# Performance work log

Measured on AMD Instinct MI355X. Metric: run time of the kernel, lower is better.

The kernel has to match this reference:

```python
import jax, jax.numpy as jnp
import numpy as np
import math

D_MODEL = 1024
NUM_HEADS = 16
D_K = D_MODEL // NUM_HEADS
MAX_SEQ_LEN = 2048
THETA = 10000.0
BATCH = 2
SEQ = 2048


def setup_inputs() -> dict:
    key = jax.random.key(0)
    ks = jax.random.split(key, 5)
    std = math.sqrt(2.0 / (D_MODEL + D_MODEL))
    def w(k):
        return jnp.clip(std * jax.random.normal(k, (D_MODEL, D_MODEL), dtype=jnp.float32), -3 * std, 3 * std)
    return {
        "x": jax.random.normal(ks[0], (BATCH, SEQ, D_MODEL), dtype=jnp.float32),
        "token_positions": jnp.arange(SEQ, dtype=jnp.int32),
        "Wq": w(ks[1]),
        "Wk": w(ks[2]),
        "Wv": w(ks[3]),
        "Wo": w(ks[4]),
    }


def _rope_tables():
    inv_freq = 1.0 / THETA ** (jnp.arange(0, D_K, 2, dtype=jnp.float32) / D_K)  # [d_k/2]
    positions = jnp.arange(MAX_SEQ_LEN, dtype=jnp.float32)[:, None]             # [max_seq, 1]
    angles = positions * inv_freq                                               # [max_seq, d_k/2]
    return jnp.cos(angles), jnp.sin(angles)


def _apply_rope(x, cos, sin):
    # x: [..., seq, d_k]; cos/sin: [seq, d_k/2] (broadcast over leading dims)
    x1, x2 = x[..., ::2], x[..., 1::2]
    r1 = x1 * cos - x2 * sin
    r2 = x1 * sin + x2 * cos
    return jnp.stack((r1, r2), axis=-1).reshape(x.shape)


def reference(x, token_positions, Wq, Wk, Wv, Wo):
    B, S, D = x.shape
    def proj(W):
        y = jnp.einsum('bsd,od->bso', x, W)
        return y.reshape(B, S, NUM_HEADS, D_K).transpose(0, 2, 1, 3)  # [B,H,S,dk]
    q, k, v = proj(Wq), proj(Wk), proj(Wv)

    cos_t, sin_t = _rope_tables()
    cos, sin = cos_t[token_positions], sin_t[token_positions]  # [S, d_k/2]
    q = _apply_rope(q, cos, sin)
    k = _apply_rope(k, cos, sin)

    scores = jnp.einsum('bhqd,bhkd->bhqk', q, k) / math.sqrt(D_K)
    causal = jnp.tril(jnp.ones((S, S), dtype=bool))
    scores = jnp.where(causal, scores, -jnp.inf)
    attn = jax.nn.softmax(scores, axis=-1)
    out = jnp.einsum('bhqk,bhkd->bhqd', attn, v)
    out = out.transpose(0, 2, 1, 3).reshape(B, S, D)
    return jnp.einsum('bsd,od->bso', out, Wo)
```

## Files before the change

### kernel.cpp

```cpp
#include <hip/hip_runtime.h>
#include <hip/hip_bf16.h>


typedef __attribute__((ext_vector_type(8))) short short8;
typedef __attribute__((ext_vector_type(4))) float floatx4;

static __device__ __forceinline__ unsigned short f2bf(float f) {
  __hip_bfloat16 h = __float2bfloat16(f);
  return *(unsigned short*)&h;
}

static __device__ __forceinline__ void gl2lds16(const unsigned short* g,
                                                unsigned short* l) {
  __builtin_amdgcn_global_load_lds(
      (const __attribute__((address_space(1))) void*)g,
      (__attribute__((address_space(3))) void*)l, 16, 0, 0);
}

__global__ __launch_bounds__(256) void cvt_all(
    const float4* __restrict__ x,  const float4* __restrict__ wq,
    const float4* __restrict__ wk, const float4* __restrict__ wv,
    const float4* __restrict__ wo,
    ushort4* __restrict__ xb,  ushort4* __restrict__ wqb,
    ushort4* __restrict__ wkb, ushort4* __restrict__ wvb,
    ushort4* __restrict__ wob,
    const int* __restrict__ tokpos,
    float* __restrict__ ctab, float* __restrict__ stab) {
  int t = blockIdx.y;
  int i = blockIdx.x * 256 + threadIdx.x;
  if (t == 5) {
    if (i < 65536) {
      int s = i >> 5, f = i & 31;
      float inv = expf(-9.210340371976184f * (float)(2 * f) / 64.0f);
      float ang = (float)tokpos[s] * inv;
      ctab[i] = cosf(ang);
      stab[i] = sinf(ang);
    }
    return;
  }
  const float4* s = (t == 0) ? x : (t == 1) ? wq : (t == 2) ? wk : (t == 3) ? wv : wo;
  ushort4* d = (t == 0) ? xb : (t == 1) ? wqb : (t == 2) ? wkb : (t == 3) ? wvb : wob;
  int n4 = (t == 0) ? 1048576 : 262144;
  if (i < n4) {
    float4 v = s[i];
    ushort4 o;
    o.x = f2bf(v.x); o.y = f2bf(v.y); o.z = f2bf(v.z); o.w = f2bf(v.w);
    d[i] = o;
  }
}

#define GEMM128_BODY(Aptr, Wptr, m0, n0)                                        \
  __shared__ __align__(16) unsigned short lA[128 * 64];                         \
  __shared__ __align__(16) unsigned short lB[128 * 64];                         \
  int tid = threadIdx.x;                                                        \
  int wave = tid >> 6, lane = tid & 63;                                         \
  int wm = wave >> 1, wn = wave & 1;                                            \
  int l15 = lane & 15, quad = lane >> 4;                                        \
  int srow = wave * 32 + (lane >> 3);                   \
  int sch = lane & 7;                                   \
  int fsw = l15 & 7;                                 \
  floatx4 acc[4][4];                                                            \
  _Pragma("unroll") for (int m = 0; m < 4; ++m)                                 \
      _Pragma("unroll") for (int n = 0; n < 4; ++n)                             \
          acc[m][n] = (floatx4){0.f, 0.f, 0.f, 0.f};                            \
  for (int kt = 0; kt < 16; ++kt) {                                             \
    _Pragma("unroll") for (int p = 0; p < 4; ++p) {                             \
      int r = srow + p * 8;                                                     \
      int g = sch ^ (r & 7);                                                    \
      gl2lds16(Aptr + (size_t)(m0 + r) * 1024 + kt * 64 + g * 8,                \
               lA + (wave * 32 + p * 8) * 64);                                  \
      gl2lds16(Wptr + (size_t)(n0 + r) * 1024 + kt * 64 + g * 8,                \
               lB + (wave * 32 + p * 8) * 64);                                  \
    }                                                                           \
    __syncthreads();                                                            \
    _Pragma("unroll") for (int ks = 0; ks < 2; ++ks) {                          \
      short8 af[4], bf[4];                                                      \
      _Pragma("unroll") for (int m = 0; m < 4; ++m)                             \
          af[m] = *(const short8*)(lA + (wm * 64 + m * 16 + l15) * 64 +         \
                                   (((ks * 4 + quad) ^ fsw) * 8));              \
      _Pragma("unroll") for (int n = 0; n < 4; ++n)                             \
          bf[n] = *(const short8*)(lB + (wn * 64 + n * 16 + l15) * 64 +         \
                                   (((ks * 4 + quad) ^ fsw) * 8));              \
      _Pragma("unroll") for (int m = 0; m < 4; ++m)                             \
          _Pragma("unroll") for (int n = 0; n < 4; ++n)                         \
              acc[m][n] = __builtin_amdgcn_mfma_f32_16x16x32_bf16(              \
                  af[m], bf[n], acc[m][n], 0, 0, 0);                            \
    }                                                                           \
    __syncthreads();                                                            \
  }

__global__ __launch_bounds__(256) void qkv_mfma(
    const unsigned short* __restrict__ X,
    const unsigned short* __restrict__ Wq,
    const unsigned short* __restrict__ Wk,
    const unsigned short* __restrict__ Wv,
    const float* __restrict__ ctab, const float* __restrict__ stab,
    unsigned short* __restrict__ Qo, unsigned short* __restrict__ Ko,
    unsigned short* __restrict__ Vo) {
  int mat = blockIdx.z;
  const unsigned short* W = (mat == 0) ? Wq : ((mat == 1) ? Wk : Wv);
  unsigned short* Out = (mat == 0) ? Qo : ((mat == 1) ? Ko : Vo);
  int m0 = blockIdx.x * 128, n0 = blockIdx.y * 128;

  GEMM128_BODY(X, W, m0, n0)

#pragma unroll
  for (int n = 0; n < 4; ++n) {
    int col = n0 + wn * 64 + n * 16 + l15;
    int h = col >> 6;
    int d = col & 63;
    int pi = d >> 1;
    bool odd = (d & 1) != 0;
    size_t hb = (size_t)h * 2048 * 64;
#pragma unroll
    for (int m = 0; m < 4; ++m) {
      int row0 = m0 + wm * 64 + m * 16 + quad * 4;
      int b = row0 >> 11;
      int s0 = row0 & 2047;
      size_t base = (size_t)b * 16 * 2048 * 64 + hb;
      if (mat == 2) {
        ushort4 pv;
        pv.x = f2bf(acc[m][n][0]);
        pv.y = f2bf(acc[m][n][1]);
        pv.z = f2bf(acc[m][n][2]);
        pv.w = f2bf(acc[m][n][3]);
        *(ushort4*)(Out + base + (size_t)d * 2048 + s0) = pv;
      } else {
#pragma unroll
        for (int i = 0; i < 4; ++i) {
          int s = s0 + i;
          float v = acc[m][n][i];
          float p = __shfl_xor(v, 1);
          float c = ctab[s * 32 + pi];
          float sn = stab[s * 32 + pi];
          float res = odd ? fmaf(p, sn, v * c) : fmaf(v, c, -p * sn);
          if (mat == 0) res *= 0.1803368801111204f;
          Out[base + (size_t)s * 64 + d] = f2bf(res);
        }
      }
    }
  }
}

__global__ __launch_bounds__(256) void oproj_mfma(
    const unsigned short* __restrict__ A, const unsigned short* __restrict__ Wo,
    float* __restrict__ Out) {
  int m0 = blockIdx.x * 128, n0 = blockIdx.y * 128;

  GEMM128_BODY(A, Wo, m0, n0)

#pragma unroll
  for (int m = 0; m < 4; ++m) {
#pragma unroll
    for (int n = 0; n < 4; ++n) {
      int col = n0 + wn * 64 + n * 16 + l15;
#pragma unroll
      for (int i = 0; i < 4; ++i) {
        int row = m0 + wm * 64 + m * 16 + quad * 4 + i;
        Out[(size_t)row * 1024 + col] = acc[m][n][i];
      }
    }
  }
}

#define LPS 72

__global__ __launch_bounds__(256) void attn_flash(
    const unsigned short* __restrict__ Q, const unsigned short* __restrict__ K,
    const unsigned short* __restrict__ Vt, unsigned short* __restrict__ Oc) {
  __shared__ __align__(16) unsigned short lK[64 * 64];
  __shared__ __align__(16) unsigned short lV[64 * 64];
  __shared__ unsigned short lP[4][16 * LPS];

  int tid = threadIdx.x;
  int wave = tid >> 6, lane = tid & 63;
  int l15 = lane & 15, quad = lane >> 4;

  int xb_ = blockIdx.x;
  int yb_ = blockIdx.y;
  int jb = yb_ >> 3, ib = yb_ & 7;
  int qtile;
  if (jb == 0)      qtile = xb_;
  else if (jb == 1) qtile = 31 - xb_;
  else if (jb == 2) qtile = (15 - xb_) & 31;
  else              qtile = (16 + xb_) & 31;
  int bh = ib * 4 + jb;

  size_t base = (size_t)bh * 2048 * 64;
  int qbase = qtile * 64;

  const unsigned short* qrow = Q + base + (size_t)(qbase + wave * 16 + l15) * 64;
  short8 qb0 = *(const short8*)(qrow + quad * 8);
  short8 qb1 = *(const short8*)(qrow + 32 + quad * 8);

  floatx4 o[4];
  float m_i = -1e30f, l_i = 0.f;
#pragma unroll
  for (int n = 0; n < 4; ++n) o[n] = (floatx4){0.f, 0.f, 0.f, 0.f};

  int r0 = tid >> 3, g = tid & 7;
  int r1 = r0 + 32;
  int e0 = g * 8;
  int sl = (g ^ (r0 & 7)) * 8;
  int fsw = l15 & 7;
  int c0 = (quad ^ fsw) * 8;
  int c1 = ((quad + 4) ^ fsw) * 8;

  const unsigned short* kp = K + base;
  const unsigned short* vp = Vt + base;
  short8 pk0 = *(const short8*)(kp + r0 * 64 + e0);
  short8 pk1 = *(const short8*)(kp + r1 * 64 + e0);
  short8 pv0 = *(const short8*)(vp + (size_t)r0 * 2048 + e0);
  short8 pv1 = *(const short8*)(vp + (size_t)r1 * 2048 + e0);

  for (int kt = 0; kt <= qtile; ++kt) {
    __syncthreads();
    *(short8*)(lK + r0 * 64 + sl) = pk0;
    *(short8*)(lK + r1 * 64 + sl) = pk1;
    *(short8*)(lV + r0 * 64 + sl) = pv0;
    *(short8*)(lV + r1 * 64 + sl) = pv1;
    __syncthreads();

    if (kt < qtile) {
      const unsigned short* kn = K + base + (size_t)(kt + 1) * 64 * 64;
      const unsigned short* vn = Vt + base + (kt + 1) * 64;
      pk0 = *(const short8*)(kn + r0 * 64 + e0);
      pk1 = *(const short8*)(kn + r1 * 64 + e0);
      pv0 = *(const short8*)(vn + (size_t)r0 * 2048 + e0);
      pv1 = *(const short8*)(vn + (size_t)r1 * 2048 + e0);
    }

    float sc[4][4];
#pragma unroll
    for (int sub = 0; sub < 4; ++sub) {
      const unsigned short* kr = lK + (sub * 16 + l15) * 64;
      short8 a0 = *(const short8*)(kr + c0);
      short8 a1 = *(const short8*)(kr + c1);
      floatx4 s = {0.f, 0.f, 0.f, 0.f};
      s = __builtin_amdgcn_mfma_f32_16x16x32_bf16(a0, qb0, s, 0, 0, 0);
      s = __builtin_amdgcn_mfma_f32_16x16x32_bf16(a1, qb1, s, 0, 0, 0);
#pragma unroll
      for (int i = 0; i < 4; ++i) sc[sub][i] = s[i];
    }

    if (kt == qtile) {
      int qin = wave * 16 + l15;
#pragma unroll
      for (int sub = 0; sub < 4; ++sub)
#pragma unroll
        for (int i = 0; i < 4; ++i)
          if (sub * 16 + quad * 4 + i > qin) sc[sub][i] = -1e30f;
    }

    float mb = sc[0][0];
#pragma unroll
    for (int sub = 0; sub < 4; ++sub)
#pragma unroll
      for (int i = 0; i < 4; ++i) mb = fmaxf(mb, sc[sub][i]);
    mb = fmaxf(mb, __shfl_xor(mb, 16));
    mb = fmaxf(mb, __shfl_xor(mb, 32));

    float mn = fmaxf(m_i, mb);
    float al = exp2f(m_i - mn);
    m_i = mn;
    float rs = 0.f;
#pragma unroll
    for (int sub = 0; sub < 4; ++sub)
#pragma unroll
      for (int i = 0; i < 4; ++i) {
        float p = exp2f(sc[sub][i] - mn);
        sc[sub][i] = p;
        rs += p;
      }
    rs += __shfl_xor(rs, 16);
    rs += __shfl_xor(rs, 32);
    l_i = l_i * al + rs;

#pragma unroll
    for (int n = 0; n < 4; ++n) {
      o[n][0] *= al; o[n][1] *= al; o[n][2] *= al; o[n][3] *= al;
    }

    unsigned short* pw = lP[wave];
#pragma unroll
    for (int sub = 0; sub < 4; ++sub) {
      ushort4 pq;
      pq.x = f2bf(sc[sub][0]); pq.y = f2bf(sc[sub][1]);
      pq.z = f2bf(sc[sub][2]); pq.w = f2bf(sc[sub][3]);
      *(ushort4*)(pw + l15 * LPS + sub * 16 + quad * 4) = pq;
    }

    const unsigned short* pr = pw + l15 * LPS + quad * 8;
    short8 pa0 = *(const short8*)(pr);
    short8 pa1 = *(const short8*)(pr + 32);

#pragma unroll
    for (int n = 0; n < 4; ++n) {
      const unsigned short* vr = lV + (n * 16 + l15) * 64;
      short8 vb0 = *(const short8*)(vr + c0);
      short8 vb1 = *(const short8*)(vr + c1);
      o[n] = __builtin_amdgcn_mfma_f32_16x16x32_bf16(vb0, pa0, o[n], 0, 0, 0);
      o[n] = __builtin_amdgcn_mfma_f32_16x16x32_bf16(vb1, pa1, o[n], 0, 0, 0);
    }
  }

  int b = bh >> 4, h = bh & 15;
  float inv = 1.f / l_i;
  int s = qbase + wave * 16 + l15;
  size_t orow = (size_t)(b * 2048 + s) * 1024 + h * 64;
#pragma unroll
  for (int n = 0; n < 4; ++n) {
    ushort4 ov;
    ov.x = f2bf(o[n][0] * inv);
    ov.y = f2bf(o[n][1] * inv);
    ov.z = f2bf(o[n][2] * inv);
    ov.w = f2bf(o[n][3] * inv);
    *(ushort4*)(Oc + orow + n * 16 + quad * 4) = ov;
  }
}

extern "C" void kernel_launch(void* const* d_in, const int* in_sizes, int n_in,
                              void* d_out, int out_size, void* d_ws, size_t ws_size,
                              hipStream_t stream) {
  const float* x  = (const float*)d_in[0];
  const int* tokpos = (const int*)d_in[1];
  const float* Wq = (const float*)d_in[2];
  const float* Wk = (const float*)d_in[3];
  const float* Wv = (const float*)d_in[4];
  const float* Wo = (const float*)d_in[5];
  float* out = (float*)d_out;

  float* ws = (float*)d_ws;
  float* ctab = ws;
  float* stab = ctab + 65536;
  unsigned short* u = (unsigned short*)(stab + 65536);
  unsigned short* Qb  = u;
  unsigned short* Kb  = Qb + 4194304;
  unsigned short* Vb  = Kb + 4194304;
  unsigned short* Oc  = Vb + 4194304;
  unsigned short* xb  = Oc + 4194304;
  unsigned short* Wqb = xb + 4194304;
  unsigned short* Wkb = Wqb + 1048576;
  unsigned short* Wvb = Wkb + 1048576;
  unsigned short* Wob = Wvb + 1048576;

  cvt_all<<<dim3(4096, 6), 256, 0, stream>>>(
      (const float4*)x, (const float4*)Wq, (const float4*)Wk,
      (const float4*)Wv, (const float4*)Wo,
      (ushort4*)xb, (ushort4*)Wqb, (ushort4*)Wkb, (ushort4*)Wvb, (ushort4*)Wob,
      tokpos, ctab, stab);

  qkv_mfma<<<dim3(32, 8, 3), 256, 0, stream>>>(
      xb, Wqb, Wkb, Wvb, ctab, stab, Qb, Kb, Vb);
  attn_flash<<<dim3(32, 32), 256, 0, stream>>>(Qb, Kb, Vb, Oc);
  oproj_mfma<<<dim3(32, 8), 256, 0, stream>>>(Oc, Wob, out);
}
```

Baseline: 203.3 us.

## Retile output projection to 64x128 blocks and speed up softmax conversions

Replaces the shared 128x128 GEMM body in the output projection with a dedicated 64x128 tile kernel. Each wave owns 32 columns and the grid doubles to 512 blocks for better CU occupancy on the 4096x1024 output. In attention, exp2f becomes raw v_exp_f32 inline asm, and bf16 packing uses a rounding-add plus perm pack in place of per-element conversions. The new bf16 rounding is not exactly round-to-nearest-even and ignores NaN handling. The new GEMM has no double-buffering, so each k-tile waits on its own loads.

```diff
diff --git a/kernel.cpp b/kernel.cpp
--- a/kernel.cpp
+++ b/kernel.cpp
@@ -8,6 +8,18 @@
 static __device__ __forceinline__ unsigned short f2bf(float f) {
   __hip_bfloat16 h = __float2bfloat16(f);
   return *(unsigned short*)&h;
+}
+
+static __device__ __forceinline__ unsigned int pk2bf(float a, float b) {
+  unsigned int ua = __float_as_uint(a) + 0x8000u;
+  unsigned int ub = __float_as_uint(b) + 0x8000u;
+  return __builtin_amdgcn_perm(ub, ua, 0x07060302u);
+}
+
+static __device__ __forceinline__ float fexp2(float x) {
+  float r;
+  asm("v_exp_f32 %0, %1\n\ts_nop 0" : "=v"(r) : "v"(x));
+  return r;
 }
 
 static __device__ __forceinline__ void gl2lds16(const unsigned short* g,
@@ -145,18 +157,65 @@
 __global__ __launch_bounds__(256) void oproj_mfma(
     const unsigned short* __restrict__ A, const unsigned short* __restrict__ Wo,
     float* __restrict__ Out) {
-  int m0 = blockIdx.x * 128, n0 = blockIdx.y * 128;
-
-  GEMM128_BODY(A, Wo, m0, n0)
+  __shared__ __align__(16) unsigned short lA[64 * 64];
+  __shared__ __align__(16) unsigned short lB[128 * 64];
+  int tid = threadIdx.x;
+  int wave = tid >> 6, lane = tid & 63;
+  int l15 = lane & 15, quad = lane >> 4;
+  int rsub = lane >> 3, sch = lane & 7;
+  int fsw = l15 & 7;
+  int m0 = blockIdx.x * 64, n0 = blockIdx.y * 128;
+
+  floatx4 acc[4][2];
+#pragma unroll
+  for (int m = 0; m < 4; ++m)
+#pragma unroll
+    for (int n = 0; n < 2; ++n) acc[m][n] = (floatx4){0.f, 0.f, 0.f, 0.f};
+
+  for (int kt = 0; kt < 16; ++kt) {
+#pragma unroll
+    for (int p = 0; p < 2; ++p) {
+      int r = wave * 16 + p * 8 + rsub;
+      int g = sch ^ (r & 7);
+      gl2lds16(A + (size_t)(m0 + r) * 1024 + kt * 64 + g * 8,
+               lA + (wave * 16 + p * 8) * 64);
+    }
+#pragma unroll
+    for (int p = 0; p < 4; ++p) {
+      int r = wave * 32 + p * 8 + rsub;
+      int g = sch ^ (r & 7);
+      gl2lds16(Wo + (size_t)(n0 + r) * 1024 + kt * 64 + g * 8,
+               lB + (wave * 32 + p * 8) * 64);
+    }
+    __syncthreads();
+#pragma unroll
+    for (int ks = 0; ks < 2; ++ks) {
+      int slot = ((ks * 4 + quad) ^ fsw) * 8;
+      short8 af[4], bf[2];
+#pragma unroll
+      for (int m = 0; m < 4; ++m)
+        af[m] = *(const short8*)(lA + (m * 16 + l15) * 64 + slot);
+#pragma unroll
+      for (int n = 0; n < 2; ++n)
+        bf[n] = *(const short8*)(lB + (wave * 32 + n * 16 + l15) * 64 + slot);
+#pragma unroll
+      for (int m = 0; m < 4; ++m)
+#pragma unroll
+        for (int n = 0; n < 2; ++n)
+          acc[m][n] = __builtin_amdgcn_mfma_f32_16x16x32_bf16(
+              af[m], bf[n], acc[m][n], 0, 0, 0);
+    }
+    __syncthreads();
+  }
 
 #pragma unroll
   for (int m = 0; m < 4; ++m) {
 #pragma unroll
-    for (int n = 0; n < 4; ++n) {
-      int col = n0 + wn * 64 + n * 16 + l15;
+    for (int n = 0; n < 2; ++n) {
+      int col = n0 + wave * 32 + n * 16 + l15;
 #pragma unroll
       for (int i = 0; i < 4; ++i) {
-        int row = m0 + wm * 64 + m * 16 + quad * 4 + i;
+        int row = m0 + m * 16 + quad * 4 + i;
         Out[(size_t)row * 1024 + col] = acc[m][n][i];
       }
     }
@@ -222,7 +281,7 @@
     __syncthreads();
 
     if (kt < qtile) {
-      const unsigned short* kn = K + base + (size_t)(kt + 1) * 64 * 64;
+      const unsigned short* kn = K + base + (size_t)(kt + 1) * 4096;
       const unsigned short* vn = Vt + base + (kt + 1) * 64;
       pk0 = *(const short8*)(kn + r0 * 64 + e0);
       pk1 = *(const short8*)(kn + r1 * 64 + e0);
@@ -261,14 +320,14 @@
     mb = fmaxf(mb, __shfl_xor(mb, 32));
 
     float mn = fmaxf(m_i, mb);
-    float al = exp2f(m_i - mn);
+    float al = fexp2(m_i - mn);
     m_i = mn;
     float rs = 0.f;
 #pragma unroll
     for (int sub = 0; sub < 4; ++sub)
 #pragma unroll
       for (int i = 0; i < 4; ++i) {
-        float p = exp2f(sc[sub][i] - mn);
+        float p = fexp2(sc[sub][i] - mn);
         sc[sub][i] = p;
         rs += p;
       }
@@ -281,16 +340,16 @@
       o[n][0] *= al; o[n][1] *= al; o[n][2] *= al; o[n][3] *= al;
     }
 
-    unsigned short* pw = lP[wave];
+    unsigned short* pw = lP[wave] + l15 * LPS;
 #pragma unroll
     for (int sub = 0; sub < 4; ++sub) {
-      ushort4 pq;
-      pq.x = f2bf(sc[sub][0]); pq.y = f2bf(sc[sub][1]);
-      pq.z = f2bf(sc[sub][2]); pq.w = f2bf(sc[sub][3]);
-      *(ushort4*)(pw + l15 * LPS + sub * 16 + quad * 4) = pq;
-    }
-
-    const unsigned short* pr = pw + l15 * LPS + quad * 8;
+      uint2 w;
+      w.x = pk2bf(sc[sub][0], sc[sub][1]);
+      w.y = pk2bf(sc[sub][2], sc[sub][3]);
+      *(uint2*)(pw + sub * 16 + quad * 4) = w;
+    }
+
+    const unsigned short* pr = lP[wave] + l15 * LPS + quad * 8;
     short8 pa0 = *(const short8*)(pr);
     short8 pa1 = *(const short8*)(pr + 32);
 
@@ -310,12 +369,10 @@
   size_t orow = (size_t)(b * 2048 + s) * 1024 + h * 64;
 #pragma unroll
   for (int n = 0; n < 4; ++n) {
-    ushort4 ov;
-    ov.x = f2bf(o[n][0] * inv);
-    ov.y = f2bf(o[n][1] * inv);
-    ov.z = f2bf(o[n][2] * inv);
-    ov.w = f2bf(o[n][3] * inv);
-    *(ushort4*)(Oc + orow + n * 16 + quad * 4) = ov;
+    uint2 ov;
+    ov.x = pk2bf(o[n][0] * inv, o[n][1] * inv);
+    ov.y = pk2bf(o[n][2] * inv, o[n][3] * inv);
+    *(uint2*)(Oc + orow + n * 16 + quad * 4) = ov;
   }
 }
 
@@ -353,5 +410,5 @@
   qkv_mfma<<<dim3(32, 8, 3), 256, 0, stream>>>(
       xb, Wqb, Wkb, Wvb, ctab, stab, Qb, Kb, Vb);
   attn_flash<<<dim3(32, 32), 256, 0, stream>>>(Qb, Kb, Vb, Oc);
-  oproj_mfma<<<dim3(32, 8), 256, 0, stream>>>(Oc, Wob, out);
-}
+  oproj_mfma<<<dim3(64, 8), 256, 0, stream>>>(Oc, Wob, out);
+}
```

Measured after the change: 190.4 us. 1.07x faster.
